# Performance work log

Hardware: AMD Instinct MI355X
Metric: run time of the kernel (lower is better)

## Reference

```python
import jax, jax.numpy as jnp
import numpy as np

N_TOK = 256
C_Z = 128
C = 32
N_HEAD = 4


def setup_inputs() -> dict:
    key = jax.random.key(0)
    ks = jax.random.split(key, 8)
    s = 0.02
    return {
        "z": jax.random.normal(ks[0], (N_TOK, N_TOK, C_Z), dtype=jnp.float32),
        "single_mask": jnp.ones((N_TOK,), dtype=jnp.float32),
        "ln_gamma": jnp.ones((C_Z,), dtype=jnp.float32),
        "ln_beta": jnp.zeros((C_Z,), dtype=jnp.float32),
        "W_q": jax.random.normal(ks[1], (C_Z, N_HEAD * C), dtype=jnp.float32) * s,
        "W_k": jax.random.normal(ks[2], (C_Z, N_HEAD * C), dtype=jnp.float32) * s,
        "W_v": jax.random.normal(ks[3], (C_Z, N_HEAD * C), dtype=jnp.float32) * s,
        "W_b": jax.random.normal(ks[4], (C_Z, N_HEAD), dtype=jnp.float32) * s,
        "W_g": jax.random.normal(ks[5], (C_Z, N_HEAD * C), dtype=jnp.float32) * s,
        "W_out": jax.random.normal(ks[6], (N_HEAD * C, C_Z), dtype=jnp.float32) * s,
    }


def reference(z, single_mask, ln_gamma, ln_beta, W_q, W_k, W_v, W_b, W_g, W_out):
    # LayerNorm over c_z
    mu = jnp.mean(z, axis=-1, keepdims=True)
    var = jnp.var(z, axis=-1, keepdims=True)
    zn = (z - mu) * jax.lax.rsqrt(var + 1e-5) * ln_gamma + ln_beta

    n = zn.shape[0]
    proj = lambda W: (zn @ W).reshape(n, n, N_HEAD, C)
    q = proj(W_q)
    k = proj(W_k)
    v = proj(W_v)
    g = proj(W_g)
    b = zn @ W_b  # [i, j, h] -> used as bias b[j, k, h]

    # a[i,j,k,h] = q[i,j]·k[i,k]/sqrt(c) + b[j,k,h]
    a = jnp.einsum('ijhc,ikhc->ijkh', q, k) / np.sqrt(C).astype(np.float32)
    a = a + b[None, :, :, :]
    a = a + (-1e9) * (1.0 - single_mask)[None, None, :, None]
    a = jax.nn.softmax(a, axis=-2)  # over k

    o = jnp.einsum('ijkh,ikhc->ijhc', a, v)
    o = jax.nn.sigmoid(g) * o
    o = o.reshape(n, n, N_HEAD * C)
    return o @ W_out
```

## Files before the change

### kernel.cpp

```cpp
#include <hip/hip_runtime.h>
#include <hip/hip_bf16.h>

#define NT 256
#define CZ 128
#define CH 32
#define NH 4
#define PL 2097152

typedef unsigned short ushort_t;
typedef unsigned int uint_t;
typedef __attribute__((ext_vector_type(8))) short short8;
typedef __attribute__((ext_vector_type(4))) float f32x4;

__device__ __forceinline__ float bfbits2f(uint_t bits){
  union { uint_t u; float f; } v; v.u = bits; return v.f;
}
__device__ __forceinline__ float bf2f(ushort_t u){
  return bfbits2f(((uint_t)u) << 16);
}
__device__ __forceinline__ ushort_t f2bf(float f){
  union { float f; uint_t u; } v; v.f = f;
  uint_t u = v.u;
  uint_t r = (u + 0x7fffu + ((u >> 16) & 1u)) >> 16;
  return (ushort_t)r;
}
__device__ __forceinline__ void unpk(uint_t w, float& lo, float& hi){
  lo = bfbits2f(w << 16);
  hi = bfbits2f(w & 0xffff0000u);
}
__device__ __forceinline__ short8 as_s8(uint4 u){
  union { uint4 u; short8 s; } v; v.u = u; return v.s;
}
__device__ __forceinline__ uint_t pk2(float a, float b){
  union { __hip_bfloat16 h; ushort_t u; } x, y;
  x.h = __float2bfloat16(a); y.h = __float2bfloat16(b);
  return (uint_t)x.u | ((uint_t)y.u << 16);
}
__device__ __forceinline__ int detect_f32(const ushort_t* zz){
  int l = threadIdx.x & 63;
  int bad = 0;
  #pragma unroll
  for(int s=0;s<4;s++){
    float v = bf2f(zz[l*4 + s]);
    if(!(fabsf(v) < 1e9f)) bad = 1;
  }
  return (__ballot(bad) != 0ull) ? 1 : 0;
}

__global__ void k_cvt_small(const void* __restrict__ m_, const void* __restrict__ g_,
    const void* __restrict__ b_, const void* __restrict__ wb_,
    float* __restrict__ dst, const ushort_t* __restrict__ zz){
  int isf32 = detect_f32(zz);
  int idx = threadIdx.x * 4;
  const void* sp; int off;
  if(idx < 256){ sp = m_;  off = idx; }
  else if(idx < 384){ sp = g_;  off = idx-256; }
  else if(idx < 512){ sp = b_;  off = idx-384; }
  else { sp = wb_; off = idx-512; }
  float4 o;
  if(isf32){ o = *(const float4*)((const float*)sp + off); }
  else {
    uint2 u = *(const uint2*)((const ushort_t*)sp + off);
    unpk(u.x, o.x, o.y); unpk(u.y, o.z, o.w);
  }
  *(float4*)(dst + idx) = o;
}

__global__ __launch_bounds__(256) void k_cvt_wt(const void* __restrict__ s0,
    const void* __restrict__ s1, const void* __restrict__ s2,
    const void* __restrict__ s3, const void* __restrict__ s4,
    ushort_t* __restrict__ dst, const ushort_t* __restrict__ zz){
  int isf32 = detect_f32(zz);
  const void* srcs[5] = {s0,s1,s2,s3,s4};
  int w = blockIdx.x >> 6;
  int idx = (blockIdx.x & 63)*256 + threadIdx.x;
  int k = idx >> 7, c = idx & 127;
  const void* sp = srcs[w];
  float v;
  if(isf32) v = ((const float*)sp)[idx];
  else      v = bf2f(((const ushort_t*)sp)[idx]);
  dst[(size_t)w*16384 + (size_t)c*128 + k] = f2bf(v);
}

__global__ __launch_bounds__(256) void k_lnproj(const void* __restrict__ zraw,
    const float* __restrict__ smallf, const ushort_t* __restrict__ Wt,
    ushort_t* __restrict__ qh, ushort_t* __restrict__ kh,
    ushort_t* __restrict__ vh, ushort_t* __restrict__ gh,
    float* __restrict__ btm){
  __shared__ __align__(16) char lds[47104];
  ushort_t* znl = (ushort_t*)lds;
  float*    tbB = (float*)(lds + 34816);
  float*    wbs = (float*)(lds + 45056);
  const float* mkf = smallf;
  const float* gmf = smallf + 256;
  const float* btf = smallf + 384;
  const float* Wbf = smallf + 512;
  int t = threadIdx.x;
  int isf32 = detect_f32((const ushort_t*)zraw);
  wbs[t] = Wbf[t]; wbs[t+256] = Wbf[t+256];
  __syncthreads();

  int row_loc = t >> 1, half = t & 1;
  size_t r = (size_t)blockIdx.x*128 + row_loc;
  float mval = -1e9f * (1.f - mkf[r & 255]);
  float s = 0.f, s2 = 0.f;
  if(isf32){
    const float4* zp = (const float4*)((const float*)zraw + r*CZ + half*64);
    #pragma unroll
    for(int q=0;q<16;q++){
      float4 v = zp[q];
      s  += (v.x + v.y) + (v.z + v.w);
      s2 += (v.x*v.x + v.y*v.y) + (v.z*v.z + v.w*v.w);
    }
  } else {
    const uint4* zp = (const uint4*)((const ushort_t*)zraw + r*CZ + half*64);
    #pragma unroll
    for(int q=0;q<8;q++){
      uint4 u = zp[q];
      const uint_t* pu = (const uint_t*)&u;
      #pragma unroll
      for(int e=0;e<4;e++){
        float lo, hi; unpk(pu[e], lo, hi);
        s += lo + hi; s2 += lo*lo + hi*hi;
      }
    }
  }
  s  += __shfl_xor(s, 1);
  s2 += __shfl_xor(s2, 1);
  float mu  = s * (1.f/CZ);
  float var = fmaxf(s2 * (1.f/CZ) - mu*mu, 0.f);
  float rs  = rsqrtf(var + 1e-5f);
  float acch[4] = {0.f,0.f,0.f,0.f};
  #pragma unroll
  for(int chunk=0;chunk<8;chunk++){
    float v8[8];
    if(isf32){
      const float4* zp = (const float4*)((const float*)zraw + r*CZ + half*64 + chunk*8);
      float4 a = zp[0], b = zp[1];
      v8[0]=a.x; v8[1]=a.y; v8[2]=a.z; v8[3]=a.w;
      v8[4]=b.x; v8[5]=b.y; v8[6]=b.z; v8[7]=b.w;
    } else {
      uint4 u = *(const uint4*)((const ushort_t*)zraw + r*CZ + half*64 + chunk*8);
      const uint_t* pu = (const uint_t*)&u;
      #pragma unroll
      for(int e=0;e<4;e++) unpk(pu[e], v8[e*2], v8[e*2+1]);
    }
    uint_t ow[4];
    #pragma unroll
    for(int e2=0;e2<4;e2++){
      int cg = half*64 + chunk*8 + e2*2;
      float v0 = (v8[e2*2]   - mu)*rs*gmf[cg]   + btf[cg];
      float v1 = (v8[e2*2+1] - mu)*rs*gmf[cg+1] + btf[cg+1];
      float4 w0 = *(const float4*)&wbs[cg*4];
      float4 w1 = *(const float4*)&wbs[(cg+1)*4];
      acch[0] += v0*w0.x + v1*w1.x;
      acch[1] += v0*w0.y + v1*w1.y;
      acch[2] += v0*w0.z + v1*w1.z;
      acch[3] += v0*w0.w + v1*w1.w;
      ow[e2] = (uint_t)f2bf(v0) | ((uint_t)f2bf(v1) << 16);
    }
    uint4 o; o.x=ow[0]; o.y=ow[1]; o.z=ow[2]; o.w=ow[3];
    *(uint4*)(znl + row_loc*136 + half*64 + chunk*8) = o;
  }
  #pragma unroll
  for(int h=0;h<4;h++){
    float tot = acch[h] + __shfl_xor(acch[h], 1);
    if(half == 0) btm[(size_t)h*65536 + r] = (tot + mval) * 1.4426950408889634f;
  }
  __syncthreads();

  int wave = t>>6, l = t&63, n = l&15, quad = l>>4;
  uint4 af[2][4];
  #pragma unroll
  for(int mt=0;mt<2;mt++)
    #pragma unroll
    for(int kb=0;kb<4;kb++)
      af[mt][kb] = *(const uint4*)(znl + (wave*32 + mt*16 + n)*136 + kb*32 + quad*8);
  float* T = tbB + wave*640;
  int rrow = l >> 1, rhalf = l & 1;
  ushort_t* outs[4] = {qh, kh, vh, gh};
  size_t row0 = (size_t)blockIdx.x*128 + wave*32;
  #pragma unroll
  for(int w=0;w<4;w++){
    const ushort_t* W = Wt + (size_t)w*16384;
    ushort_t* D = outs[w];
    float sc = (w==0) ? (0.17677669529663687f * 1.4426950408889634f) : 1.f;
    #pragma unroll
    for(int nt=0;nt<8;nt++){
      uint4 bfr[4];
      #pragma unroll
      for(int kb=0;kb<4;kb++)
        bfr[kb] = *(const uint4*)(W + ((size_t)(nt*16 + n))*128 + kb*32 + quad*8);
      f32x4 a0 = {0.f,0.f,0.f,0.f}, a1 = {0.f,0.f,0.f,0.f};
      #pragma unroll
      for(int kb=0;kb<4;kb++){
        a0 = __builtin_amdgcn_mfma_f32_16x16x32_bf16(as_s8(af[0][kb]), as_s8(bfr[kb]), a0, 0,0,0);
        a1 = __builtin_amdgcn_mfma_f32_16x16x32_bf16(as_s8(af[1][kb]), as_s8(bfr[kb]), a1, 0,0,0);
      }
      #pragma unroll
      for(int rr=0;rr<4;rr++){
        T[(quad*4 + rr)*20 + n]      = a0[rr];
        T[(16 + quad*4 + rr)*20 + n] = a1[rr];
      }
      float4 v0 = *(const float4*)(T + rrow*20 + rhalf*8);
      float4 v1 = *(const float4*)(T + rrow*20 + rhalf*8 + 4);
      uint4 o;
      o.x = (uint_t)f2bf(v0.x*sc) | ((uint_t)f2bf(v0.y*sc) << 16);
      o.y = (uint_t)f2bf(v0.z*sc) | ((uint_t)f2bf(v0.w*sc) << 16);
      o.z = (uint_t)f2bf(v1.x*sc) | ((uint_t)f2bf(v1.y*sc) << 16);
      o.w = (uint_t)f2bf(v1.z*sc) | ((uint_t)f2bf(v1.w*sc) << 16);
      *(uint4*)(D + (size_t)(nt>>1)*PL + (row0 + rrow)*CH + (nt&1)*16 + rhalf*8) = o;
    }
  }
}

__global__ __launch_bounds__(256, 2) void k_attn(
    const ushort_t* __restrict__ qh, const ushort_t* __restrict__ kh,
    const ushort_t* __restrict__ vh, const ushort_t* __restrict__ gh,
    const float* __restrict__ btm, ushort_t* __restrict__ oh){
  __shared__ __align__(16) char lds[40960];
  uint4*    VfA = (uint4*)lds;
  uint4*    Kf  = (uint4*)(lds + 16384);
  ushort_t* Pw0 = (ushort_t*)(lds + 32768);
  int t = threadIdx.x;
  int i = blockIdx.x >> 2, h = blockIdx.x & 3;
  int wave = t >> 6, l = t & 63;
  int n = l & 15, quad = l >> 4;
  const ushort_t* qhp = qh + (size_t)h*PL + (size_t)(i*NT)*CH;
  const ushort_t* khp = kh + (size_t)h*PL + (size_t)(i*NT)*CH;
  const ushort_t* vhp = vh + (size_t)h*PL + (size_t)(i*NT)*CH;
  const ushort_t* ghp = gh + (size_t)h*PL + (size_t)(i*NT)*CH;
  ushort_t*       ohp = oh + (size_t)h*PL + (size_t)(i*NT)*CH;
  const float*    bth = btm + (size_t)h*65536;

  {
    #pragma unroll
    for(int m=0;m<4;m++){
      int kt = wave*4 + m;
      Kf[kt*64 + l] = *(const uint4*)(khp + (size_t)(kt*16 + n)*CH + quad*8);
    }
  }
  {
    #pragma unroll
    for(int it=0; it<4; it++){
      int u = wave + it*4, kblk = u >> 1, ct = u & 1;
      uint_t d[4];
      #pragma unroll
      for(int e=0;e<4;e++){
        uint_t lo = vhp[(size_t)(kblk*32 + quad*8 + e*2    )*CH + ct*16 + n];
        uint_t hi = vhp[(size_t)(kblk*32 + quad*8 + e*2 + 1)*CH + ct*16 + n];
        d[e] = lo | (hi << 16);
      }
      uint4 o; o.x=d[0]; o.y=d[1]; o.z=d[2]; o.w=d[3];
      VfA[u*64 + l] = o;
    }
  }
  __syncthreads();

  ushort_t* Pw = Pw0 + wave*1024;
  int swz = (n & 7) << 4;

  #pragma unroll 1
  for(int s=0;s<4;s++){
    int jt = wave*4 + s;
    uint4 qf = *(const uint4*)(qhp + (size_t)(jt*16 + n)*CH + quad*8);
    f32x4 acc[16];
    #pragma unroll
    for(int kt=0;kt<16;kt++)
      acc[kt] = *(const f32x4*)(bth + (size_t)(jt*16 + n)*256 + kt*16 + quad*4);
    #pragma unroll
    for(int kt=0;kt<16;kt++){
      uint4 kfv = Kf[kt*64 + l];
      acc[kt] = __builtin_amdgcn_mfma_f32_16x16x32_bf16(as_s8(kfv), as_s8(qf), acc[kt], 0,0,0);
    }
    float sum0 = 0.f, sum1 = 0.f;
    f32x4 oa0 = {0.f,0.f,0.f,0.f}, oa1 = {0.f,0.f,0.f,0.f};
    #pragma unroll
    for(int H=0;H<2;H++){
      uint2 pv[8];
      #pragma unroll
      for(int kt=0;kt<8;kt++){
        float e0 = __builtin_amdgcn_exp2f(acc[H*8+kt][0]);
        float e1 = __builtin_amdgcn_exp2f(acc[H*8+kt][1]);
        float e2 = __builtin_amdgcn_exp2f(acc[H*8+kt][2]);
        float e3 = __builtin_amdgcn_exp2f(acc[H*8+kt][3]);
        sum0 += e0 + e1; sum1 += e2 + e3;
        pv[kt].x = pk2(e0, e1);
        pv[kt].y = pk2(e2, e3);
      }
      #pragma unroll
      for(int Q2=0;Q2<2;Q2++){
        #pragma unroll
        for(int m=0;m<4;m++)
          *(uint2*)((char*)Pw + (((n<<7) + (m<<5) + (quad<<3)) ^ swz)) = pv[Q2*4+m];
        #pragma unroll
        for(int kb=0;kb<2;kb++){
          uint4 pf = *(const uint4*)((char*)Pw + (((n<<7) + (kb<<6) + (quad<<4)) ^ swz));
          int kg = (H*2+Q2)*2 + kb;
          oa0 = __builtin_amdgcn_mfma_f32_16x16x32_bf16(as_s8(VfA[(kg*2+0)*64 + l]), as_s8(pf), oa0, 0,0,0);
          oa1 = __builtin_amdgcn_mfma_f32_16x16x32_bf16(as_s8(VfA[(kg*2+1)*64 + l]), as_s8(pf), oa1, 0,0,0);
        }
      }
    }
    float ssum = sum0 + sum1;
    ssum += __shfl_xor(ssum, 16);
    ssum += __shfl_xor(ssum, 32);
    float inv = 1.f / ssum;
    size_t rb = (size_t)(jt*16 + n)*CH;
    uint2 g0 = *(const uint2*)(ghp + rb + quad*4);
    uint2 g1 = *(const uint2*)(ghp + rb + 16 + quad*4);
    float ga[4], gc[4];
    unpk(g0.x, ga[0], ga[1]); unpk(g0.y, ga[2], ga[3]);
    unpk(g1.x, gc[0], gc[1]); unpk(g1.y, gc[2], gc[3]);
    float v0[4], v1[4];
    #pragma unroll
    for(int rr=0;rr<4;rr++){
      v0[rr] = oa0[rr] * inv * (1.f/(1.f + __expf(-ga[rr])));
      v1[rr] = oa1[rr] * inv * (1.f/(1.f + __expf(-gc[rr])));
    }
    uint2 s0, s1;
    s0.x = (uint_t)f2bf(v0[0]) | ((uint_t)f2bf(v0[1]) << 16);
    s0.y = (uint_t)f2bf(v0[2]) | ((uint_t)f2bf(v0[3]) << 16);
    s1.x = (uint_t)f2bf(v1[0]) | ((uint_t)f2bf(v1[1]) << 16);
    s1.y = (uint_t)f2bf(v1[2]) | ((uint_t)f2bf(v1[3]) << 16);
    *(uint2*)(ohp + rb + quad*4)      = s0;
    *(uint2*)(ohp + rb + 16 + quad*4) = s1;
  }
}

__global__ __launch_bounds__(256) void k_gemm1(const ushort_t* __restrict__ oh,
    const ushort_t* __restrict__ Wt, void* __restrict__ outp,
    const ushort_t* __restrict__ zz){
  __shared__ __align__(16) float tbB[4*640];
  int isf32 = detect_f32(zz);
  int t = threadIdx.x, wave = t>>6, l = t&63, n = l&15, quad = l>>4;
  size_t row0 = (size_t)blockIdx.x*128 + wave*32;
  float* T = tbB + wave*640;
  int rrow = l >> 1, rhalf = l & 1;
  uint4 af[2][4];
  #pragma unroll
  for(int mt=0;mt<2;mt++)
    #pragma unroll
    for(int kb=0;kb<4;kb++)
      af[mt][kb] = *(const uint4*)(oh + (size_t)kb*PL + (row0 + mt*16 + n)*CH + quad*8);
  #pragma unroll
  for(int nt=0;nt<8;nt++){
    uint4 bfr[4];
    #pragma unroll
    for(int kb=0;kb<4;kb++)
      bfr[kb] = *(const uint4*)(Wt + ((size_t)(nt*16 + n))*128 + kb*32 + quad*8);
    f32x4 a0 = {0.f,0.f,0.f,0.f}, a1 = {0.f,0.f,0.f,0.f};
    #pragma unroll
    for(int kb=0;kb<4;kb++){
      a0 = __builtin_amdgcn_mfma_f32_16x16x32_bf16(as_s8(af[0][kb]), as_s8(bfr[kb]), a0, 0,0,0);
      a1 = __builtin_amdgcn_mfma_f32_16x16x32_bf16(as_s8(af[1][kb]), as_s8(bfr[kb]), a1, 0,0,0);
    }
    #pragma unroll
    for(int rr=0;rr<4;rr++){
      T[(quad*4 + rr)*20 + n]      = a0[rr];
      T[(16 + quad*4 + rr)*20 + n] = a1[rr];
    }
    float4 v0 = *(const float4*)(T + rrow*20 + rhalf*8);
    float4 v1 = *(const float4*)(T + rrow*20 + rhalf*8 + 4);
    if(isf32){
      float* of = (float*)outp + (row0 + rrow)*CZ + nt*16 + rhalf*8;
      *(float4*)of = v0;
      *(float4*)(of + 4) = v1;
    } else {
      uint4 o;
      o.x = (uint_t)f2bf(v0.x) | ((uint_t)f2bf(v0.y) << 16);
      o.y = (uint_t)f2bf(v0.z) | ((uint_t)f2bf(v0.w) << 16);
      o.z = (uint_t)f2bf(v1.x) | ((uint_t)f2bf(v1.y) << 16);
      o.w = (uint_t)f2bf(v1.z) | ((uint_t)f2bf(v1.w) << 16);
      *(uint4*)((ushort_t*)outp + (row0 + rrow)*CZ + nt*16 + rhalf*8) = o;
    }
  }
}

extern "C" void kernel_launch(void* const* d_in, const int* in_sizes, int n_in,
                              void* d_out, int out_size, void* d_ws, size_t ws_size,
                              hipStream_t stream){
  char* wsb = (char*)d_ws;
  const size_t TB = (size_t)16777216;
  ushort_t* qh  = (ushort_t*)(wsb);
  ushort_t* kh  = (ushort_t*)(wsb + TB);
  ushort_t* vh  = (ushort_t*)(wsb + 2*TB);
  ushort_t* gh  = (ushort_t*)(wsb + 3*TB);
  ushort_t* oh  = (ushort_t*)(wsb + 4*TB);
  float*    btm = (float*)   (wsb + 5*TB);
  float*  smallf= (float*)   (wsb + 5*TB + (1u<<20));
  ushort_t* Wt  = (ushort_t*)(wsb + 5*TB + (1u<<20) + 4096);
  const ushort_t* zz = (const ushort_t*)d_in[0];

  k_cvt_small<<<1,   256, 0, stream>>>(d_in[1], d_in[2], d_in[3], d_in[7], smallf, zz);
  k_cvt_wt   <<<320, 256, 0, stream>>>(d_in[4], d_in[5], d_in[6], d_in[8], d_in[9], Wt, zz);
  k_lnproj   <<<512, 256, 0, stream>>>(d_in[0], smallf, Wt, qh, kh, vh, gh, btm);
  k_attn     <<<1024,256, 0, stream>>>(qh, kh, vh, gh, btm, oh);
  k_gemm1    <<<512, 256, 0, stream>>>(oh, Wt + (size_t)4*16384, d_out, zz);
}
```

Baseline: 212.5 us.

## Halve rows per LN-projection block and split projections across wave pairs

The LayerNorm+projection kernel now processes 64 rows per block instead of 128, with four threads per row, and launches twice as many blocks. Each pair of waves shares 32 rows, and each wave computes two of the four projection outputs instead of all four. Each thread loads its z values once into registers rather than reading z twice. LDS drops from about 47KB to 30KB and the padded row stride changes to 140, which is meant to raise occupancy and parallelism. In exchange each weight tile is read by more blocks and register pressure rises from the 32-element register array.

New measurement: 211.8 us. Within noise of the previous version (-0.4%).

```diff
diff --git a/kernel.cpp b/kernel.cpp
--- a/kernel.cpp
+++ b/kernel.cpp
@@ -87,10 +87,10 @@
     ushort_t* __restrict__ qh, ushort_t* __restrict__ kh,
     ushort_t* __restrict__ vh, ushort_t* __restrict__ gh,
     float* __restrict__ btm){
-  __shared__ __align__(16) char lds[47104];
+  __shared__ __align__(16) char lds[30208];
   ushort_t* znl = (ushort_t*)lds;
-  float*    tbB = (float*)(lds + 34816);
-  float*    wbs = (float*)(lds + 45056);
+  float*    tbB = (float*)(lds + 17920);
+  float*    wbs = (float*)(lds + 28160);
   const float* mkf = smallf;
   const float* gmf = smallf + 256;
   const float* btf = smallf + 384;
@@ -100,57 +100,45 @@
   wbs[t] = Wbf[t]; wbs[t+256] = Wbf[t+256];
   __syncthreads();
 
-  int row_loc = t >> 1, half = t & 1;
-  size_t r = (size_t)blockIdx.x*128 + row_loc;
+  int rl = t >> 2, q4 = t & 3;
+  size_t r = (size_t)blockIdx.x*64 + rl;
   float mval = -1e9f * (1.f - mkf[r & 255]);
-  float s = 0.f, s2 = 0.f;
+  float v[32];
   if(isf32){
-    const float4* zp = (const float4*)((const float*)zraw + r*CZ + half*64);
-    #pragma unroll
-    for(int q=0;q<16;q++){
-      float4 v = zp[q];
-      s  += (v.x + v.y) + (v.z + v.w);
-      s2 += (v.x*v.x + v.y*v.y) + (v.z*v.z + v.w*v.w);
+    const float4* zp = (const float4*)((const float*)zraw + r*CZ + q4*32);
+    #pragma unroll
+    for(int q=0;q<8;q++){
+      float4 x = zp[q];
+      v[q*4]=x.x; v[q*4+1]=x.y; v[q*4+2]=x.z; v[q*4+3]=x.w;
     }
   } else {
-    const uint4* zp = (const uint4*)((const ushort_t*)zraw + r*CZ + half*64);
-    #pragma unroll
-    for(int q=0;q<8;q++){
+    const uint4* zp = (const uint4*)((const ushort_t*)zraw + r*CZ + q4*32);
+    #pragma unroll
+    for(int q=0;q<4;q++){
       uint4 u = zp[q];
       const uint_t* pu = (const uint_t*)&u;
       #pragma unroll
-      for(int e=0;e<4;e++){
-        float lo, hi; unpk(pu[e], lo, hi);
-        s += lo + hi; s2 += lo*lo + hi*hi;
-      }
-    }
-  }
-  s  += __shfl_xor(s, 1);
-  s2 += __shfl_xor(s2, 1);
+      for(int e=0;e<4;e++) unpk(pu[e], v[q*8+e*2], v[q*8+e*2+1]);
+    }
+  }
+  float s = 0.f, s2 = 0.f;
+  #pragma unroll
+  for(int j=0;j<32;j++){ s += v[j]; s2 += v[j]*v[j]; }
+  s  += __shfl_xor(s, 1);  s2 += __shfl_xor(s2, 1);
+  s  += __shfl_xor(s, 2);  s2 += __shfl_xor(s2, 2);
   float mu  = s * (1.f/CZ);
   float var = fmaxf(s2 * (1.f/CZ) - mu*mu, 0.f);
   float rs  = rsqrtf(var + 1e-5f);
   float acch[4] = {0.f,0.f,0.f,0.f};
   #pragma unroll
-  for(int chunk=0;chunk<8;chunk++){
-    float v8[8];
-    if(isf32){
-      const float4* zp = (const float4*)((const float*)zraw + r*CZ + half*64 + chunk*8);
-      float4 a = zp[0], b = zp[1];
-      v8[0]=a.x; v8[1]=a.y; v8[2]=a.z; v8[3]=a.w;
-      v8[4]=b.x; v8[5]=b.y; v8[6]=b.z; v8[7]=b.w;
-    } else {
-      uint4 u = *(const uint4*)((const ushort_t*)zraw + r*CZ + half*64 + chunk*8);
-      const uint_t* pu = (const uint_t*)&u;
-      #pragma unroll
-      for(int e=0;e<4;e++) unpk(pu[e], v8[e*2], v8[e*2+1]);
-    }
+  for(int chunk=0;chunk<4;chunk++){
     uint_t ow[4];
     #pragma unroll
     for(int e2=0;e2<4;e2++){
-      int cg = half*64 + chunk*8 + e2*2;
-      float v0 = (v8[e2*2]   - mu)*rs*gmf[cg]   + btf[cg];
-      float v1 = (v8[e2*2+1] - mu)*rs*gmf[cg+1] + btf[cg+1];
+      int idx = chunk*8 + e2*2;
+      int cg  = q4*32 + idx;
+      float v0 = (v[idx]   - mu)*rs*gmf[cg]   + btf[cg];
+      float v1 = (v[idx+1] - mu)*rs*gmf[cg+1] + btf[cg+1];
       float4 w0 = *(const float4*)&wbs[cg*4];
       float4 w1 = *(const float4*)&wbs[(cg+1)*4];
       acch[0] += v0*w0.x + v1*w1.x;
@@ -160,28 +148,32 @@
       ow[e2] = (uint_t)f2bf(v0) | ((uint_t)f2bf(v1) << 16);
     }
     uint4 o; o.x=ow[0]; o.y=ow[1]; o.z=ow[2]; o.w=ow[3];
-    *(uint4*)(znl + row_loc*136 + half*64 + chunk*8) = o;
-  }
-  #pragma unroll
-  for(int h=0;h<4;h++){
-    float tot = acch[h] + __shfl_xor(acch[h], 1);
-    if(half == 0) btm[(size_t)h*65536 + r] = (tot + mval) * 1.4426950408889634f;
+    *(uint4*)(znl + rl*140 + q4*32 + chunk*8) = o;
+  }
+  #pragma unroll
+  for(int hh=0;hh<4;hh++){
+    float tot = acch[hh];
+    tot += __shfl_xor(tot, 1);
+    tot += __shfl_xor(tot, 2);
+    if(q4 == 0) btm[(size_t)hh*65536 + r] = (tot + mval) * 1.4426950408889634f;
   }
   __syncthreads();
 
   int wave = t>>6, l = t&63, n = l&15, quad = l>>4;
+  int wg = wave >> 1, wsel = wave & 1;
   uint4 af[2][4];
   #pragma unroll
   for(int mt=0;mt<2;mt++)
     #pragma unroll
     for(int kb=0;kb<4;kb++)
-      af[mt][kb] = *(const uint4*)(znl + (wave*32 + mt*16 + n)*136 + kb*32 + quad*8);
+      af[mt][kb] = *(const uint4*)(znl + (wg*32 + mt*16 + n)*140 + kb*32 + quad*8);
   float* T = tbB + wave*640;
   int rrow = l >> 1, rhalf = l & 1;
   ushort_t* outs[4] = {qh, kh, vh, gh};
-  size_t row0 = (size_t)blockIdx.x*128 + wave*32;
-  #pragma unroll
-  for(int w=0;w<4;w++){
+  size_t row0 = (size_t)blockIdx.x*64 + wg*32;
+  #pragma unroll
+  for(int ww=0;ww<2;ww++){
+    int w = wsel*2 + ww;
     const ushort_t* W = Wt + (size_t)w*16384;
     ushort_t* D = outs[w];
     float sc = (w==0) ? (0.17677669529663687f * 1.4426950408889634f) : 1.f;
@@ -394,7 +386,7 @@
 
   k_cvt_small<<<1,   256, 0, stream>>>(d_in[1], d_in[2], d_in[3], d_in[7], smallf, zz);
   k_cvt_wt   <<<320, 256, 0, stream>>>(d_in[4], d_in[5], d_in[6], d_in[8], d_in[9], Wt, zz);
-  k_lnproj   <<<512, 256, 0, stream>>>(d_in[0], smallf, Wt, qh, kh, vh, gh, btm);
+  k_lnproj   <<<1024,256, 0, stream>>>(d_in[0], smallf, Wt, qh, kh, vh, gh, btm);
   k_attn     <<<1024,256, 0, stream>>>(qh, kh, vh, gh, btm, oh);
   k_gemm1    <<<512, 256, 0, stream>>>(oh, Wt + (size_t)4*16384, d_out, zz);
 }
```

## Merge small conversion kernel into weight conversion and drop LDS transpose in GEMMs

Applied to the files above, without the earlier changes.

Folds the single-block small-parameter conversion into the weight-conversion launch as an extra block, removing one kernel launch. In both projection GEMMs the MFMA operands are swapped so the accumulator comes out transposed. Results are then stored directly from registers as narrower 8/16-byte writes, with no round trip through an LDS staging tile. The znl row stride is also padded from 136 to 140 elements to change LDS bank mapping. The cost is smaller, less coalesced global stores in exchange for fewer LDS accesses and less LDS per block.

Result: no change. 209.7 us (-1.3%).

```diff
diff --git a/kernel.cpp b/kernel.cpp
--- a/kernel.cpp
+++ b/kernel.cpp
@@ -47,30 +47,30 @@
   return (__ballot(bad) != 0ull) ? 1 : 0;
 }
 
-__global__ void k_cvt_small(const void* __restrict__ m_, const void* __restrict__ g_,
-    const void* __restrict__ b_, const void* __restrict__ wb_,
-    float* __restrict__ dst, const ushort_t* __restrict__ zz){
-  int isf32 = detect_f32(zz);
-  int idx = threadIdx.x * 4;
-  const void* sp; int off;
-  if(idx < 256){ sp = m_;  off = idx; }
-  else if(idx < 384){ sp = g_;  off = idx-256; }
-  else if(idx < 512){ sp = b_;  off = idx-384; }
-  else { sp = wb_; off = idx-512; }
-  float4 o;
-  if(isf32){ o = *(const float4*)((const float*)sp + off); }
-  else {
-    uint2 u = *(const uint2*)((const ushort_t*)sp + off);
-    unpk(u.x, o.x, o.y); unpk(u.y, o.z, o.w);
-  }
-  *(float4*)(dst + idx) = o;
-}
-
 __global__ __launch_bounds__(256) void k_cvt_wt(const void* __restrict__ s0,
     const void* __restrict__ s1, const void* __restrict__ s2,
     const void* __restrict__ s3, const void* __restrict__ s4,
-    ushort_t* __restrict__ dst, const ushort_t* __restrict__ zz){
+    ushort_t* __restrict__ dst, const ushort_t* __restrict__ zz,
+    const void* __restrict__ m_, const void* __restrict__ g_,
+    const void* __restrict__ b_, const void* __restrict__ wb_,
+    float* __restrict__ smallf){
   int isf32 = detect_f32(zz);
+  if(blockIdx.x >= 320){
+    int idx = threadIdx.x * 4;
+    const void* sp; int off;
+    if(idx < 256){ sp = m_;  off = idx; }
+    else if(idx < 384){ sp = g_;  off = idx-256; }
+    else if(idx < 512){ sp = b_;  off = idx-384; }
+    else { sp = wb_; off = idx-512; }
+    float4 o;
+    if(isf32){ o = *(const float4*)((const float*)sp + off); }
+    else {
+      uint2 u = *(const uint2*)((const ushort_t*)sp + off);
+      unpk(u.x, o.x, o.y); unpk(u.y, o.z, o.w);
+    }
+    *(float4*)(smallf + idx) = o;
+    return;
+  }
   const void* srcs[5] = {s0,s1,s2,s3,s4};
   int w = blockIdx.x >> 6;
   int idx = (blockIdx.x & 63)*256 + threadIdx.x;
@@ -87,10 +87,9 @@
     ushort_t* __restrict__ qh, ushort_t* __restrict__ kh,
     ushort_t* __restrict__ vh, ushort_t* __restrict__ gh,
     float* __restrict__ btm){
-  __shared__ __align__(16) char lds[47104];
+  __shared__ __align__(16) char lds[37888];
   ushort_t* znl = (ushort_t*)lds;
-  float*    tbB = (float*)(lds + 34816);
-  float*    wbs = (float*)(lds + 45056);
+  float*    wbs = (float*)(lds + 35840);
   const float* mkf = smallf;
   const float* gmf = smallf + 256;
   const float* btf = smallf + 384;
@@ -160,7 +159,7 @@
       ow[e2] = (uint_t)f2bf(v0) | ((uint_t)f2bf(v1) << 16);
     }
     uint4 o; o.x=ow[0]; o.y=ow[1]; o.z=ow[2]; o.w=ow[3];
-    *(uint4*)(znl + row_loc*136 + half*64 + chunk*8) = o;
+    *(uint4*)(znl + row_loc*140 + half*64 + chunk*8) = o;
   }
   #pragma unroll
   for(int h=0;h<4;h++){
@@ -175,9 +174,7 @@
   for(int mt=0;mt<2;mt++)
     #pragma unroll
     for(int kb=0;kb<4;kb++)
-      af[mt][kb] = *(const uint4*)(znl + (wave*32 + mt*16 + n)*136 + kb*32 + quad*8);
-  float* T = tbB + wave*640;
-  int rrow = l >> 1, rhalf = l & 1;
+      af[mt][kb] = *(const uint4*)(znl + (wave*32 + mt*16 + n)*140 + kb*32 + quad*8);
   ushort_t* outs[4] = {qh, kh, vh, gh};
   size_t row0 = (size_t)blockIdx.x*128 + wave*32;
   #pragma unroll
@@ -194,22 +191,15 @@
       f32x4 a0 = {0.f,0.f,0.f,0.f}, a1 = {0.f,0.f,0.f,0.f};
       #pragma unroll
       for(int kb=0;kb<4;kb++){
-        a0 = __builtin_amdgcn_mfma_f32_16x16x32_bf16(as_s8(af[0][kb]), as_s8(bfr[kb]), a0, 0,0,0);
-        a1 = __builtin_amdgcn_mfma_f32_16x16x32_bf16(as_s8(af[1][kb]), as_s8(bfr[kb]), a1, 0,0,0);
-      }
-      #pragma unroll
-      for(int rr=0;rr<4;rr++){
-        T[(quad*4 + rr)*20 + n]      = a0[rr];
-        T[(16 + quad*4 + rr)*20 + n] = a1[rr];
-      }
-      float4 v0 = *(const float4*)(T + rrow*20 + rhalf*8);
-      float4 v1 = *(const float4*)(T + rrow*20 + rhalf*8 + 4);
-      uint4 o;
-      o.x = (uint_t)f2bf(v0.x*sc) | ((uint_t)f2bf(v0.y*sc) << 16);
-      o.y = (uint_t)f2bf(v0.z*sc) | ((uint_t)f2bf(v0.w*sc) << 16);
-      o.z = (uint_t)f2bf(v1.x*sc) | ((uint_t)f2bf(v1.y*sc) << 16);
-      o.w = (uint_t)f2bf(v1.z*sc) | ((uint_t)f2bf(v1.w*sc) << 16);
-      *(uint4*)(D + (size_t)(nt>>1)*PL + (row0 + rrow)*CH + (nt&1)*16 + rhalf*8) = o;
+        a0 = __builtin_amdgcn_mfma_f32_16x16x32_bf16(as_s8(bfr[kb]), as_s8(af[0][kb]), a0, 0,0,0);
+        a1 = __builtin_amdgcn_mfma_f32_16x16x32_bf16(as_s8(bfr[kb]), as_s8(af[1][kb]), a1, 0,0,0);
+      }
+      uint2 s0p, s1p;
+      s0p.x = pk2(a0[0]*sc, a0[1]*sc); s0p.y = pk2(a0[2]*sc, a0[3]*sc);
+      s1p.x = pk2(a1[0]*sc, a1[1]*sc); s1p.y = pk2(a1[2]*sc, a1[3]*sc);
+      ushort_t* Db = D + (size_t)(nt>>1)*PL + (size_t)(nt&1)*16 + quad*4;
+      *(uint2*)(Db + (row0 + n)*CH)      = s0p;
+      *(uint2*)(Db + (row0 + 16 + n)*CH) = s1p;
     }
   }
 }
@@ -331,12 +321,9 @@
 __global__ __launch_bounds__(256) void k_gemm1(const ushort_t* __restrict__ oh,
     const ushort_t* __restrict__ Wt, void* __restrict__ outp,
     const ushort_t* __restrict__ zz){
-  __shared__ __align__(16) float tbB[4*640];
   int isf32 = detect_f32(zz);
   int t = threadIdx.x, wave = t>>6, l = t&63, n = l&15, quad = l>>4;
   size_t row0 = (size_t)blockIdx.x*128 + wave*32;
-  float* T = tbB + wave*640;
-  int rrow = l >> 1, rhalf = l & 1;
   uint4 af[2][4];
   #pragma unroll
   for(int mt=0;mt<2;mt++)
@@ -352,27 +339,20 @@
     f32x4 a0 = {0.f,0.f,0.f,0.f}, a1 = {0.f,0.f,0.f,0.f};
     #pragma unroll
     for(int kb=0;kb<4;kb++){
-      a0 = __builtin_amdgcn_mfma_f32_16x16x32_bf16(as_s8(af[0][kb]), as_s8(bfr[kb]), a0, 0,0,0);
-      a1 = __builtin_amdgcn_mfma_f32_16x16x32_bf16(as_s8(af[1][kb]), as_s8(bfr[kb]), a1, 0,0,0);
-    }
-    #pragma unroll
-    for(int rr=0;rr<4;rr++){
-      T[(quad*4 + rr)*20 + n]      = a0[rr];
-      T[(16 + quad*4 + rr)*20 + n] = a1[rr];
-    }
-    float4 v0 = *(const float4*)(T + rrow*20 + rhalf*8);
-    float4 v1 = *(const float4*)(T + rrow*20 + rhalf*8 + 4);
+      a0 = __builtin_amdgcn_mfma_f32_16x16x32_bf16(as_s8(bfr[kb]), as_s8(af[0][kb]), a0, 0,0,0);
+      a1 = __builtin_amdgcn_mfma_f32_16x16x32_bf16(as_s8(bfr[kb]), as_s8(af[1][kb]), a1, 0,0,0);
+    }
     if(isf32){
-      float* of = (float*)outp + (row0 + rrow)*CZ + nt*16 + rhalf*8;
-      *(float4*)of = v0;
-      *(float4*)(of + 4) = v1;
+      float* of = (float*)outp + nt*16 + quad*4;
+      *(f32x4*)(of + (row0 + n)*CZ)      = a0;
+      *(f32x4*)(of + (row0 + 16 + n)*CZ) = a1;
     } else {
-      uint4 o;
-      o.x = (uint_t)f2bf(v0.x) | ((uint_t)f2bf(v0.y) << 16);
-      o.y = (uint_t)f2bf(v0.z) | ((uint_t)f2bf(v0.w) << 16);
-      o.z = (uint_t)f2bf(v1.x) | ((uint_t)f2bf(v1.y) << 16);
-      o.w = (uint_t)f2bf(v1.z) | ((uint_t)f2bf(v1.w) << 16);
-      *(uint4*)((ushort_t*)outp + (row0 + rrow)*CZ + nt*16 + rhalf*8) = o;
+      uint2 s0p, s1p;
+      s0p.x = pk2(a0[0], a0[1]); s0p.y = pk2(a0[2], a0[3]);
+      s1p.x = pk2(a1[0], a1[1]); s1p.y = pk2(a1[2], a1[3]);
+      ushort_t* ob = (ushort_t*)outp + nt*16 + quad*4;
+      *(uint2*)(ob + (row0 + n)*CZ)      = s0p;
+      *(uint2*)(ob + (row0 + 16 + n)*CZ) = s1p;
     }
   }
 }
@@ -392,8 +372,8 @@
   ushort_t* Wt  = (ushort_t*)(wsb + 5*TB + (1u<<20) + 4096);
   const ushort_t* zz = (const ushort_t*)d_in[0];
 
-  k_cvt_small<<<1,   256, 0, stream>>>(d_in[1], d_in[2], d_in[3], d_in[7], smallf, zz);
-  k_cvt_wt   <<<320, 256, 0, stream>>>(d_in[4], d_in[5], d_in[6], d_in[8], d_in[9], Wt, zz);
+  k_cvt_wt   <<<321, 256, 0, stream>>>(d_in[4], d_in[5], d_in[6], d_in[8], d_in[9],
+                                       Wt, zz, d_in[1], d_in[2], d_in[3], d_in[7], smallf);
   k_lnproj   <<<512, 256, 0, stream>>>(d_in[0], smallf, Wt, qh, kh, vh, gh, btm);
   k_attn     <<<1024,256, 0, stream>>>(qh, kh, vh, gh, btm, oh);
   k_gemm1    <<<512, 256, 0, stream>>>(oh, Wt + (size_t)4*16384, d_out, zz);
```
